# Optimization experiments

Hardware: AMD Instinct MI355X
Metric: run time of the kernel (lower is better)

Reference implementation:

```python
import jax, jax.numpy as jnp
import numpy as np

N_COORD = 4
VB = 1.0
N_WALKERS = 2_000_000


def setup_inputs() -> dict:
    key = jax.random.key(0)
    Rs = jax.random.normal(key, (N_WALKERS, N_COORD, 3), dtype=jnp.float32)
    A = (2.0 / VB) * jnp.ones((N_COORD,), dtype=jnp.float32)
    C = jnp.ones((N_COORD,), dtype=jnp.complex64)
    return {"Rs": Rs, "A": A, "C": C}


def _psi_and_nabla(Rs, A, C):
    # hydrogenic product ansatz: psi = sum_n C_n * prod_k exp(-r_k / A_n)
    r = jnp.sqrt(jnp.sum(Rs * Rs, axis=-1))          # [W, K] radii
    r_sum = jnp.sum(r, axis=-1)                      # [W]
    invr_sum = jnp.sum(1.0 / r, axis=-1)             # [W]
    e = jnp.exp(-r_sum[:, None] / A[None, :])        # [W, N] real
    psi = jnp.einsum('wn,n->w', e, C)                # complex64 [W]
    # Laplacian of exp(-r/a) per particle: (1/a^2 - 2/(a r)) * exp(-r/a)
    lap = (N_COORD / (A * A))[None, :] - (2.0 / A)[None, :] * invr_sum[:, None]
    nabla_psi = jnp.einsum('wn,n->w', e * lap, C)    # [W]
    return psi, nabla_psi


def reference(Rs, A, C):
    psi, nabla_psi = _psi_and_nabla(Rs, A, C)
    # all-pairs Coulomb: V = -VB * sum_{a<b} 1/|r_a - r_b|
    ia, ib = np.triu_indices(N_COORD, k=1)
    diff = Rs[:, ia, :] - Rs[:, ib, :]               # [W, P, 3]
    dist = jnp.sqrt(jnp.sum(diff * diff, axis=-1))   # [W, P]
    V = -VB * jnp.sum(1.0 / dist, axis=-1)           # [W]
    K_psi = -0.5 * nabla_psi
    H_psi = K_psi + V.astype(psi.dtype) * psi
    psistar = jnp.conj(psi)
    return psistar * H_psi / (VB ** 2), jnp.abs(psistar) ** 2
```

## Files before the change

kernel.cpp:

```cpp
#include <hip/hip_runtime.h>

#define NC  4
#define TPB 256
#define WPT 2
#define WPB (TPB * WPT)

__global__ __launch_bounds__(TPB) void wvfn_kernel(
    const float* __restrict__ Rs,
    const float* __restrict__ A,
    const float* __restrict__ C,
    float* __restrict__ out,
    int W)
{
    __shared__ float4 sh[WPB * 3];

    const int t = threadIdx.x;
    const size_t blk_first_q = (size_t)blockIdx.x * (WPB * 3);
    const size_t total_q     = (size_t)W * 3;

    const float4* g = (const float4*)Rs;
    #pragma unroll
    for (int k = 0; k < 3 * WPT; ++k) {
        size_t q = blk_first_q + t + (size_t)k * TPB;
        if (q < total_q) sh[t + k * TPB] = g[q];
    }

    float invA[NC], lap1[NC], lap2[NC], cre[NC];
    #pragma unroll
    for (int n = 0; n < NC; ++n) {
        float ia = 1.0f / A[n];
        invA[n] = ia;
        lap1[n] = (float)NC * ia * ia;
        lap2[n] = 2.0f * ia;
        cre[n]  = C[n];
    }

    __syncthreads();

    #pragma unroll
    for (int u = 0; u < WPT; ++u) {
        const int li = t + u * TPB;
        const int w  = blockIdx.x * WPB + li;
        if (w >= W) break;

        float4 q0 = sh[3 * li + 0];
        float4 q1 = sh[3 * li + 1];
        float4 q2 = sh[3 * li + 2];

        float x0 = q0.x, y0 = q0.y, z0 = q0.z;
        float x1 = q0.w, y1 = q1.x, z1 = q1.y;
        float x2 = q1.z, y2 = q1.w, z2 = q2.x;
        float x3 = q2.y, y3 = q2.z, z3 = q2.w;

        float d0 = x0*x0 + y0*y0 + z0*z0;
        float d1 = x1*x1 + y1*y1 + z1*z1;
        float d2 = x2*x2 + y2*y2 + z2*z2;
        float d3 = x3*x3 + y3*y3 + z3*z3;

        float i0 = rsqrtf(d0), i1 = rsqrtf(d1), i2 = rsqrtf(d2), i3 = rsqrtf(d3);
        float r_sum    = d0*i0 + d1*i1 + d2*i2 + d3*i3;
        float invr_sum = i0 + i1 + i2 + i3;

        float V;
        {
            float dx, dy, dz, dd, s = 0.0f;
            dx = x0-x1; dy = y0-y1; dz = z0-z1; dd = dx*dx+dy*dy+dz*dz; s += rsqrtf(dd);
            dx = x0-x2; dy = y0-y2; dz = z0-z2; dd = dx*dx+dy*dy+dz*dz; s += rsqrtf(dd);
            dx = x0-x3; dy = y0-y3; dz = z0-z3; dd = dx*dx+dy*dy+dz*dz; s += rsqrtf(dd);
            dx = x1-x2; dy = y1-y2; dz = z1-z2; dd = dx*dx+dy*dy+dz*dz; s += rsqrtf(dd);
            dx = x1-x3; dy = y1-y3; dz = z1-z3; dd = dx*dx+dy*dy+dz*dz; s += rsqrtf(dd);
            dx = x2-x3; dy = y2-y3; dz = z2-z3; dd = dx*dx+dy*dy+dz*dz; s += rsqrtf(dd);
            V = -s;
        }

        float psi = 0.0f, nab = 0.0f;
        #pragma unroll
        for (int n = 0; n < NC; ++n) {
            float e   = expf(-r_sum * invA[n]);
            float lap = lap1[n] - lap2[n] * invr_sum;
            psi += cre[n] * e;
            nab += cre[n] * e * lap;
        }

        float H = -0.5f * nab + V * psi;

        __builtin_nontemporal_store(psi * H,   &out[w]);
        __builtin_nontemporal_store(psi * psi, &out[(size_t)W + w]);
    }
}

extern "C" void kernel_launch(void* const* d_in, const int* in_sizes, int n_in,
                              void* d_out, int out_size, void* d_ws, size_t ws_size,
                              hipStream_t stream) {
    const float* Rs = (const float*)d_in[0];
    const float* A  = (const float*)d_in[1];
    const float* C  = (const float*)d_in[2];
    float* out = (float*)d_out;

    int W = in_sizes[0] / 12;
    int grid = (W + WPB - 1) / WPB;
    wvfn_kernel<<<grid, TPB, 0, stream>>>(Rs, A, C, out, W);
}
```

Measured before the change: 25.00 us.

## Use persistent blocks with double-buffered global_load_lds prefetch of walker coordinates

Replaces the one-shot grid with a fixed grid of persistent blocks that loop over 256-walker chunks. Each block prefetches the next chunk straight into LDS with global_load_lds while it computes the current one, using vmcnt waits and barriers to synchronise. The aim is to hide global-load latency in this bandwidth-bound kernel and avoid register staging. The cost is hand-written waitcnt logic, extra barriers per chunk, and a hardcoded grid size that may not suit every device.

Result: slower. 25.95 us (+3.8%).

```diff
diff --git a/kernel.cpp b/kernel.cpp
--- a/kernel.cpp
+++ b/kernel.cpp
@@ -1,29 +1,45 @@
 #include <hip/hip_runtime.h>
 
-#define NC  4
-#define TPB 256
-#define WPT 2
-#define WPB (TPB * WPT)
+#define NC      4
+#define TPB     256
+#define CHUNK_W 256
+#define CHUNK_B (CHUNK_W * 48)
+#define CHUNK_Q (CHUNK_W * 3)
 
 __global__ __launch_bounds__(TPB) void wvfn_kernel(
     const float* __restrict__ Rs,
     const float* __restrict__ A,
     const float* __restrict__ C,
     float* __restrict__ out,
-    int W)
+    int W, int nchunks)
 {
-    __shared__ float4 sh[WPB * 3];
+    __shared__ float4 sh[2 * CHUNK_Q];
 
-    const int t = threadIdx.x;
-    const size_t blk_first_q = (size_t)blockIdx.x * (WPB * 3);
-    const size_t total_q     = (size_t)W * 3;
+    const int t    = threadIdx.x;
+    const int lane = t & 63;
+    const int wv   = t >> 6;
+    const size_t total_b = (size_t)W * 48;
+    const char*  gbase   = (const char*)Rs;
 
-    const float4* g = (const float4*)Rs;
-    #pragma unroll
-    for (int k = 0; k < 3 * WPT; ++k) {
-        size_t q = blk_first_q + t + (size_t)k * TPB;
-        if (q < total_q) sh[t + k * TPB] = g[q];
-    }
+    auto stage = [&](int b, int c) {
+        const size_t cb = (size_t)c * CHUNK_B;
+        #pragma unroll
+        for (int k = 0; k < 3; ++k) {
+            const int    r  = k * 4 + wv;
+            const size_t go = cb + (size_t)r * 1024;
+            if (go < total_b) {
+                const char* gp = gbase + go + (size_t)lane * 16;
+                char*       lp = (char*)sh + (size_t)b * CHUNK_B + (size_t)r * 1024;
+                __builtin_amdgcn_global_load_lds(
+                    (const __attribute__((address_space(1))) void*)gp,
+                    (__attribute__((address_space(3))) void*)lp,
+                    16, 0, 0);
+            }
+        }
+    };
+    auto full3 = [&](int c) -> bool {
+        return (size_t)c * CHUNK_B + (size_t)(8 + wv) * 1024 < total_b;
+    };
 
     float invA[NC], lap1[NC], lap2[NC], cre[NC];
     #pragma unroll
@@ -35,57 +51,70 @@
         cre[n]  = C[n];
     }
 
-    __syncthreads();
+    const int c0     = blockIdx.x;
+    const int stride = gridDim.x;
+    int cur = 0;
 
-    #pragma unroll
-    for (int u = 0; u < WPT; ++u) {
-        const int li = t + u * TPB;
-        const int w  = blockIdx.x * WPB + li;
-        if (w >= W) break;
+    if (c0 < nchunks) stage(0, c0);
 
-        float4 q0 = sh[3 * li + 0];
-        float4 q1 = sh[3 * li + 1];
-        float4 q2 = sh[3 * li + 2];
+    for (int c = c0; c < nchunks; c += stride) {
+        const int nxt = c + stride;
+        const bool have_nxt = (nxt < nchunks);
+        if (have_nxt) stage(cur ^ 1, nxt);
 
-        float x0 = q0.x, y0 = q0.y, z0 = q0.z;
-        float x1 = q0.w, y1 = q1.x, z1 = q1.y;
-        float x2 = q1.z, y2 = q1.w, z2 = q2.x;
-        float x3 = q2.y, y3 = q2.z, z3 = q2.w;
+        if (have_nxt && full3(nxt)) asm volatile("s_waitcnt vmcnt(3)" ::: "memory");
+        else                        asm volatile("s_waitcnt vmcnt(0)" ::: "memory");
+        __builtin_amdgcn_s_barrier();
 
-        float d0 = x0*x0 + y0*y0 + z0*z0;
-        float d1 = x1*x1 + y1*y1 + z1*z1;
-        float d2 = x2*x2 + y2*y2 + z2*z2;
-        float d3 = x3*x3 + y3*y3 + z3*z3;
+        const int w = c * CHUNK_W + t;
+        if (w < W) {
+            const int base = cur * CHUNK_Q + 3 * t;
+            float4 q0 = sh[base + 0];
+            float4 q1 = sh[base + 1];
+            float4 q2 = sh[base + 2];
 
-        float i0 = rsqrtf(d0), i1 = rsqrtf(d1), i2 = rsqrtf(d2), i3 = rsqrtf(d3);
-        float r_sum    = d0*i0 + d1*i1 + d2*i2 + d3*i3;
-        float invr_sum = i0 + i1 + i2 + i3;
+            float x0 = q0.x, y0 = q0.y, z0 = q0.z;
+            float x1 = q0.w, y1 = q1.x, z1 = q1.y;
+            float x2 = q1.z, y2 = q1.w, z2 = q2.x;
+            float x3 = q2.y, y3 = q2.z, z3 = q2.w;
 
-        float V;
-        {
-            float dx, dy, dz, dd, s = 0.0f;
-            dx = x0-x1; dy = y0-y1; dz = z0-z1; dd = dx*dx+dy*dy+dz*dz; s += rsqrtf(dd);
-            dx = x0-x2; dy = y0-y2; dz = z0-z2; dd = dx*dx+dy*dy+dz*dz; s += rsqrtf(dd);
-            dx = x0-x3; dy = y0-y3; dz = z0-z3; dd = dx*dx+dy*dy+dz*dz; s += rsqrtf(dd);
-            dx = x1-x2; dy = y1-y2; dz = z1-z2; dd = dx*dx+dy*dy+dz*dz; s += rsqrtf(dd);
-            dx = x1-x3; dy = y1-y3; dz = z1-z3; dd = dx*dx+dy*dy+dz*dz; s += rsqrtf(dd);
-            dx = x2-x3; dy = y2-y3; dz = z2-z3; dd = dx*dx+dy*dy+dz*dz; s += rsqrtf(dd);
-            V = -s;
+            float d0 = x0*x0 + y0*y0 + z0*z0;
+            float d1 = x1*x1 + y1*y1 + z1*z1;
+            float d2 = x2*x2 + y2*y2 + z2*z2;
+            float d3 = x3*x3 + y3*y3 + z3*z3;
+
+            float i0 = rsqrtf(d0), i1 = rsqrtf(d1), i2 = rsqrtf(d2), i3 = rsqrtf(d3);
+            float r_sum    = d0*i0 + d1*i1 + d2*i2 + d3*i3;
+            float invr_sum = i0 + i1 + i2 + i3;
+
+            float V;
+            {
+                float dx, dy, dz, dd, s = 0.0f;
+                dx = x0-x1; dy = y0-y1; dz = z0-z1; dd = dx*dx+dy*dy+dz*dz; s += rsqrtf(dd);
+                dx = x0-x2; dy = y0-y2; dz = z0-z2; dd = dx*dx+dy*dy+dz*dz; s += rsqrtf(dd);
+                dx = x0-x3; dy = y0-y3; dz = z0-z3; dd = dx*dx+dy*dy+dz*dz; s += rsqrtf(dd);
+                dx = x1-x2; dy = y1-y2; dz = z1-z2; dd = dx*dx+dy*dy+dz*dz; s += rsqrtf(dd);
+                dx = x1-x3; dy = y1-y3; dz = z1-z3; dd = dx*dx+dy*dy+dz*dz; s += rsqrtf(dd);
+                dx = x2-x3; dy = y2-y3; dz = z2-z3; dd = dx*dx+dy*dy+dz*dz; s += rsqrtf(dd);
+                V = -s;
+            }
+
+            float psi = 0.0f, nab = 0.0f;
+            #pragma unroll
+            for (int n = 0; n < NC; ++n) {
+                float e   = expf(-r_sum * invA[n]);
+                float lap = lap1[n] - lap2[n] * invr_sum;
+                psi += cre[n] * e;
+                nab += cre[n] * e * lap;
+            }
+
+            float H = -0.5f * nab + V * psi;
+            __builtin_nontemporal_store(psi * H,   &out[w]);
+            __builtin_nontemporal_store(psi * psi, &out[(size_t)W + w]);
         }
 
-        float psi = 0.0f, nab = 0.0f;
-        #pragma unroll
-        for (int n = 0; n < NC; ++n) {
-            float e   = expf(-r_sum * invA[n]);
-            float lap = lap1[n] - lap2[n] * invr_sum;
-            psi += cre[n] * e;
-            nab += cre[n] * e * lap;
-        }
-
-        float H = -0.5f * nab + V * psi;
-
-        __builtin_nontemporal_store(psi * H,   &out[w]);
-        __builtin_nontemporal_store(psi * psi, &out[(size_t)W + w]);
+        __builtin_amdgcn_s_barrier();
+        cur ^= 1;
     }
 }
 
@@ -98,6 +127,8 @@
     float* out = (float*)d_out;
 
     int W = in_sizes[0] / 12;
-    int grid = (W + WPB - 1) / WPB;
-    wvfn_kernel<<<grid, TPB, 0, stream>>>(Rs, A, C, out, W);
+    int nchunks = (W + CHUNK_W - 1) / CHUNK_W;
+    int grid = 1536;
+    if (grid > nchunks) grid = nchunks;
+    wvfn_kernel<<<grid, TPB, 0, stream>>>(Rs, A, C, out, W, nchunks);
 }
```
